# Optimization experiments

Hardware: AMD Instinct MI355X
Metric: run time of the kernel (lower is better)

## Reference

```python
import math
import jax, jax.numpy as jnp
import numpy as np

POS_DIM = 16
MLP_HIDDEN = 32
HIDDEN = 1024


def _pos_emb(n_bins: int, pos_dim: int = POS_DIM) -> jnp.ndarray:
    pos = jnp.arange(n_bins, dtype=jnp.float32)[:, None]            # [n_bins, 1]
    inv_freq = jnp.exp(jnp.arange(0, pos_dim, 2, dtype=jnp.float32)
                       * (-math.log(10000.0) / pos_dim))            # [pos_dim//2]
    pe = jnp.zeros((n_bins, pos_dim), dtype=jnp.float32)
    pe = pe.at[:, 0::2].set(jnp.sin(pos * inv_freq))
    pe = pe.at[:, 1::2].set(jnp.cos(pos * inv_freq))
    return pe


def setup_inputs() -> dict:
    key = jax.random.key(0)
    kx, k1, k2, k3, k4 = jax.random.split(key, 5)
    x = jax.random.normal(kx, (4, 4096, HIDDEN), dtype=jnp.float32)
    # filter MLP params (torch Linear default-ish init scale)
    W1 = jax.random.normal(k1, (POS_DIM, MLP_HIDDEN), dtype=jnp.float32) / math.sqrt(POS_DIM)
    b1 = jax.random.normal(k2, (MLP_HIDDEN,), dtype=jnp.float32) * 0.01
    W2 = jax.random.normal(k3, (MLP_HIDDEN, HIDDEN), dtype=jnp.float32) / math.sqrt(MLP_HIDDEN)
    b2 = jax.random.normal(k4, (HIDDEN,), dtype=jnp.float32) * 0.01
    amp_gain = jnp.ones((HIDDEN,), dtype=jnp.float32)
    return {"x": x, "W1": W1, "b1": b1, "W2": W2, "b2": b2, "amp_gain": amp_gain}


def reference(x, W1, b1, W2, b2, amp_gain):
    B, T, D = x.shape
    n_bins = T // 2 + 1
    pe = _pos_emb(n_bins)                                           # [n_bins, pos_dim]
    # tiny filter MLP: Linear -> SiLU -> Linear
    h = jax.nn.silu(pe @ W1 + b1)                                   # [n_bins, mlp_hidden]
    H = (h @ W2 + b2).astype(jnp.float32)                           # [n_bins, D]
    Xf = jnp.fft.rfft(x.astype(jnp.float32), axis=1)                # [B, n_bins, D] complex
    Yf = Xf * H[None, :, :]
    y = jnp.fft.irfft(Yf, n=T, axis=1)                              # [B, T, D]
    return y.astype(x.dtype) * amp_gain[None, None, :]
```

## Files before the change

### kernel.cpp

```cpp
#include <hip/hip_runtime.h>
#include <hip/hip_bf16.h>
#include <cstddef>


#define B_ 4
#define T_ 4096
#define D_ 1024
#define D2_ 512
#define NBINS 2049

constexpr float WC16[8] = {1.f, 0.9238795325112867f, 0.7071067811865476f,
                           0.3826834323650898f, 0.f, -0.3826834323650898f,
                           -0.7071067811865476f, -0.9238795325112867f};
constexpr float WS16[8] = {0.f, 0.3826834323650898f, 0.7071067811865476f,
                           0.9238795325112867f, 1.f, 0.9238795325112867f,
                           0.7071067811865476f, 0.3826834323650898f};

template <int SGN>
__device__ __forceinline__ void dft16(float (&vr)[16], float (&vi)[16]) {
#pragma unroll
  for (int i = 0; i < 16; ++i) {
    const int j = ((i & 1) << 3) | ((i & 2) << 1) | ((i & 4) >> 1) | ((i & 8) >> 3);
    if (j > i) {
      float t = vr[i]; vr[i] = vr[j]; vr[j] = t;
      t = vi[i]; vi[i] = vi[j]; vi[j] = t;
    }
  }
#pragma unroll
  for (int s = 1; s <= 4; ++s) {
    const int L = 1 << s, hh = L >> 1, step = 16 >> s;
#pragma unroll
    for (int k0 = 0; k0 < 16; k0 += L)
#pragma unroll
      for (int j = 0; j < hh; ++j) {
        const float wr = WC16[j * step];
        const float wi = (float)SGN * WS16[j * step];
        const int ia = k0 + j, ib = ia + hh;
        const float tr = wr * vr[ib] - wi * vi[ib];
        const float ti = wr * vi[ib] + wi * vr[ib];
        vr[ib] = vr[ia] - tr; vi[ib] = vi[ia] - ti;
        vr[ia] += tr; vi[ia] += ti;
      }
  }
}

__device__ __forceinline__ void twiddle(float& xr, float& xi, float ang) {
  float sn, cs;
  __sincosf(ang, &sn, &cs);
  const float r = xr * cs - xi * sn;
  xi = xr * sn + xi * cs;
  xr = r;
}

__global__ void k_filter_h(const float* __restrict__ W1, const float* __restrict__ b1,
                           float* __restrict__ h) {
  const int bin = blockIdx.x * 256 + threadIdx.x;
  if (bin >= NBINS) return;
  constexpr float invf[8] = {1.0f, 0.31622776601683794f, 0.1f, 0.031622776601683794f,
                             0.01f, 3.1622776601683794e-3f, 1.0e-3f, 3.1622776601683794e-4f};
  float pe[16];
#pragma unroll
  for (int i = 0; i < 8; ++i) {
    const float a = (float)bin * invf[i];
    pe[2 * i] = sinf(a);
    pe[2 * i + 1] = cosf(a);
  }
#pragma unroll
  for (int m = 0; m < 32; ++m) {
    float s = b1[m];
#pragma unroll
    for (int i = 0; i < 16; ++i) s += pe[i] * W1[i * 32 + m];
    h[bin * 32 + m] = s / (1.0f + expf(-s));
  }
}

__global__ void k_filter_HT(const float* __restrict__ h, const float* __restrict__ W2,
                            const float* __restrict__ b2, float2* __restrict__ HT) {
  const int bin = blockIdx.x * 256 + threadIdx.x;
  const int g = blockIdx.y;
  if (bin >= NBINS) return;
  float sA = b2[2 * g], sB = b2[2 * g + 1];
#pragma unroll
  for (int m = 0; m < 32; ++m) {
    const float hv = h[bin * 32 + m];
    sA += hv * W2[m * D_ + 2 * g];
    sB += hv * W2[m * D_ + 2 * g + 1];
  }
  constexpr float sc = 0.5f / 4096.0f;
  HT[(size_t)g * NBINS + bin] = make_float2((sA + sB) * sc, (sA - sB) * sc);
}

__global__ __launch_bounds__(256, 8) void k_pack_t(const float2* __restrict__ x2,
                                                   float2* __restrict__ Z) {
  __shared__ float2 tile[64][33];
  const int tid = threadIdx.x;
  const int g0 = blockIdx.x * 32;
  const int t0 = blockIdx.y * 64;
  const int b = blockIdx.z;
#pragma unroll
  for (int it = 0; it < 8; ++it) {
    const int l = tid + 256 * it;
    const int r = l >> 5, c = l & 31;
    tile[r][c] = x2[((size_t)b * T_ + t0 + r) * D2_ + g0 + c];
  }
  __syncthreads();
#pragma unroll
  for (int it = 0; it < 8; ++it) {
    const int l = tid + 256 * it;
    const int gg = l >> 6, tt = l & 63;
    Z[((size_t)b * D2_ + g0 + gg) * T_ + t0 + tt] = tile[tt][gg];
  }
}

__global__ __launch_bounds__(256, 4) void k_fft_fused(float2* __restrict__ Z,
                                                      const float2* __restrict__ HT) {
  __shared__ float2 S[4096];
  const int tid = threadIdx.x;
  const int g = blockIdx.x;
  const int b = blockIdx.y;
  float2* __restrict__ Zrow = Z + ((size_t)b * D2_ + g) * T_;
  const float2* __restrict__ HTg = HT + (size_t)g * NBINS;
  constexpr float C1f = -6.28318530717958647692f / 4096.0f;
  constexpr float C2f = -6.28318530717958647692f / 256.0f;
  constexpr float C1i = 6.28318530717958647692f / 4096.0f;
  constexpr float C2i = 6.28318530717958647692f / 256.0f;

  float vr[16], vi[16];
  {
    const int j = tid;
#pragma unroll
    for (int a = 0; a < 16; ++a) {
      const float2 t = Zrow[j + 256 * a];
      vr[a] = t.x; vi[a] = t.y;
    }
    dft16<-1>(vr, vi);
#pragma unroll
    for (int r = 1; r < 16; ++r) twiddle(vr[r], vi[r], C1f * (float)(r * j));
#pragma unroll
    for (int r = 0; r < 16; ++r) S[256 * r + j] = make_float2(vr[r], vi[r]);
  }
  __syncthreads();
  const int rr = tid >> 4, ii = tid & 15;
  {
#pragma unroll
    for (int a = 0; a < 16; ++a) {
      const float2 t = S[256 * rr + ii + 16 * a];
      vr[a] = t.x; vi[a] = t.y;
    }
    __syncthreads();
    dft16<-1>(vr, vi);
#pragma unroll
    for (int r2 = 1; r2 < 16; ++r2) twiddle(vr[r2], vi[r2], C2f * (float)(r2 * ii));
#pragma unroll
    for (int r2 = 0; r2 < 16; ++r2)
      S[256 * ii + 16 * rr + (r2 ^ ii)] = make_float2(vr[r2], vi[r2]);
  }
  __syncthreads();
  {
#pragma unroll
    for (int i2 = 0; i2 < 16; ++i2) {
      const float2 t = S[256 * i2 + 16 * rr + (ii ^ i2)];
      vr[i2] = t.x; vi[i2] = t.y;
    }
    __syncthreads();
    dft16<-1>(vr, vi);
  }
  float2 hv[16];
  {
#pragma unroll
    for (int s2 = 0; s2 < 16; ++s2) {
      const int k = rr + 16 * ii + 256 * s2;
      const int km = (k <= 2048) ? k : 4096 - k;
      hv[s2] = HTg[km];
    }
#pragma unroll
    for (int s2 = 0; s2 < 16; ++s2)
      S[256 * s2 + 16 * ii + (rr ^ ii)] = make_float2(vr[s2], vi[s2]);
    __syncthreads();
#pragma unroll
    for (int s2 = 0; s2 < 16; ++s2) {
      const int k = rr + 16 * ii + 256 * s2;
      const int kp = (4096 - k) & 4095;
      const int d0 = kp & 15, d1 = (kp >> 4) & 15, d2 = kp >> 8;
      const float2 xp = S[256 * d2 + 16 * d1 + (d0 ^ d1)];
      const float yr = hv[s2].x * vr[s2] + hv[s2].y * xp.x;
      const float yi = hv[s2].x * vi[s2] - hv[s2].y * xp.y;
      vr[s2] = yr; vi[s2] = yi;
    }
  }
  __syncthreads();
  {
    dft16<1>(vr, vi);
#pragma unroll
    for (int j0 = 1; j0 < 16; ++j0) twiddle(vr[j0], vi[j0], C2i * (float)(ii * j0));
#pragma unroll
    for (int j0 = 0; j0 < 16; ++j0)
      S[256 * j0 + 16 * rr + (ii ^ j0)] = make_float2(vr[j0], vi[j0]);
  }
  __syncthreads();
  {
#pragma unroll
    for (int r2 = 0; r2 < 16; ++r2) {
      const float2 t = S[256 * ii + 16 * rr + (r2 ^ ii)];
      vr[r2] = t.x; vi[r2] = t.y;
    }
    __syncthreads();
    dft16<1>(vr, vi);
#pragma unroll
    for (int j1 = 0; j1 < 16; ++j1)
      twiddle(vr[j1], vi[j1], C1i * (float)(rr * (ii + 16 * j1)));
#pragma unroll
    for (int j1 = 0; j1 < 16; ++j1)
      S[256 * rr + ii + 16 * j1] = make_float2(vr[j1], vi[j1]);
  }
  __syncthreads();
  {
    const int j = tid;
#pragma unroll
    for (int r = 0; r < 16; ++r) {
      const float2 t = S[256 * r + j];
      vr[r] = t.x; vi[r] = t.y;
    }
    dft16<1>(vr, vi);
#pragma unroll
    for (int a = 0; a < 16; ++a) Zrow[j + 256 * a] = make_float2(vr[a], vi[a]);
  }
}

__global__ __launch_bounds__(256, 8) void k_unpack_t(const float2* __restrict__ Z,
                                                     const float2* __restrict__ amp2,
                                                     float2* __restrict__ y2) {
  __shared__ float2 tile[64][33];
  const int tid = threadIdx.x;
  const int g0 = blockIdx.x * 32;
  const int t0 = blockIdx.y * 64;
  const int b = blockIdx.z;
#pragma unroll
  for (int it = 0; it < 8; ++it) {
    const int l = tid + 256 * it;
    const int gg = l >> 6, tt = l & 63;
    tile[tt][gg] = Z[((size_t)b * D2_ + g0 + gg) * T_ + t0 + tt];
  }
  __syncthreads();
#pragma unroll
  for (int it = 0; it < 8; ++it) {
    const int l = tid + 256 * it;
    const int r = l >> 5, c = l & 31;
    const float2 t = tile[r][c];
    const float2 av = amp2[g0 + c];
    y2[((size_t)b * T_ + t0 + r) * D2_ + g0 + c] = make_float2(t.x * av.x, t.y * av.y);
  }
}

extern "C" void kernel_launch(void* const* d_in, const int* in_sizes, int n_in,
                              void* d_out, int out_size, void* d_ws, size_t ws_size,
                              hipStream_t stream) {
  const float* x = (const float*)d_in[0];
  const float* W1 = (const float*)d_in[1];
  const float* b1 = (const float*)d_in[2];
  const float* W2 = (const float*)d_in[3];
  const float* b2 = (const float*)d_in[4];
  const float* amp = (const float*)d_in[5];
  float* out = (float*)d_out;

  float2* Z = (float2*)d_ws;
  float2* HT = (float2*)((char*)d_ws + (size_t)B_ * D2_ * T_ * sizeof(float2));
  float* h = (float*)((char*)HT + (size_t)D2_ * NBINS * sizeof(float2));

  k_filter_h<<<dim3((NBINS + 255) / 256), 256, 0, stream>>>(W1, b1, h);
  k_filter_HT<<<dim3((NBINS + 255) / 256, D2_), 256, 0, stream>>>(h, W2, b2, HT);
  k_pack_t<<<dim3(D2_ / 32, T_ / 64, B_), 256, 0, stream>>>((const float2*)x, Z);
  k_fft_fused<<<dim3(D2_, B_), 256, 0, stream>>>(Z, HT);
  k_unpack_t<<<dim3(D2_ / 32, T_ / 64, B_), 256, 0, stream>>>(Z, (const float2*)amp,
                                                              (float2*)out);
}
```

Baseline: 120.3 us.

## Chain twiddle recurrences, pre-permute filter table, reorder FFT grid for filter reuse

Twiddle factors in the FFT stages are now produced by one sincos followed by complex-multiply recurrences, replacing a sincos per element. The filter table is expanded into a per-thread pre-permuted 4096-entry layout so each FFT block reads it with coalesced loads and no index math. The FFT grid is swapped so the four batches sharing a filter row run next to each other, improving cache reuse. The 1/N scale moves into the unpack kernel. The recurrences can accumulate some float rounding error, and the filter table is larger.

New measurement: 155.1 us. 1.29x slower.

```diff
diff --git a/kernel.cpp b/kernel.cpp
--- a/kernel.cpp
+++ b/kernel.cpp
@@ -1,6 +1,7 @@
 #include <hip/hip_runtime.h>
 #include <hip/hip_bf16.h>
 #include <cstddef>
+#include <cstdint>
 
 
 #define B_ 4
@@ -44,12 +45,22 @@
   }
 }
 
-__device__ __forceinline__ void twiddle(float& xr, float& xi, float ang) {
-  float sn, cs;
-  __sincosf(ang, &sn, &cs);
-  const float r = xr * cs - xi * sn;
-  xi = xr * sn + xi * cs;
-  xr = r;
+__device__ __forceinline__ void chain_twiddle(float (&vr)[16], float (&vi)[16],
+                                              int r0, float wc, float ws) {
+  float ar = wc, ai = ws;
+#pragma unroll
+  for (int r = 1; r < 16; ++r) {
+    if (r >= r0) {
+      const float tr = vr[r] * ar - vi[r] * ai;
+      vi[r] = vr[r] * ai + vi[r] * ar;
+      vr[r] = tr;
+    }
+    if (r < 15) {
+      const float nr = ar * wc - ai * ws;
+      const float ni = ar * ws + ai * wc;
+      ar = nr; ai = ni;
+    }
+  }
 }
 
 __global__ void k_filter_h(const float* __restrict__ W1, const float* __restrict__ b1,
@@ -74,20 +85,21 @@
   }
 }
 
-__global__ void k_filter_HT(const float* __restrict__ h, const float* __restrict__ W2,
-                            const float* __restrict__ b2, float2* __restrict__ HT) {
-  const int bin = blockIdx.x * 256 + threadIdx.x;
+__global__ void k_filter_HTS(const float* __restrict__ h, const float* __restrict__ W2,
+                             const float* __restrict__ b2, float2* __restrict__ HTS) {
+  const int q = blockIdx.x * 256 + threadIdx.x;
   const int g = blockIdx.y;
-  if (bin >= NBINS) return;
+  const int tid = q & 255, s2 = q >> 8;
+  const int k = (tid >> 4) + 16 * (tid & 15) + 256 * s2;
+  const int km = (k <= 2048) ? k : 4096 - k;
   float sA = b2[2 * g], sB = b2[2 * g + 1];
 #pragma unroll
   for (int m = 0; m < 32; ++m) {
-    const float hv = h[bin * 32 + m];
+    const float hv = h[km * 32 + m];
     sA += hv * W2[m * D_ + 2 * g];
     sB += hv * W2[m * D_ + 2 * g + 1];
   }
-  constexpr float sc = 0.5f / 4096.0f;
-  HT[(size_t)g * NBINS + bin] = make_float2((sA + sB) * sc, (sA - sB) * sc);
+  HTS[(size_t)g * 4096 + q] = make_float2((sA + sB) * 0.5f, (sA - sB) * 0.5f);
 }
 
 __global__ __launch_bounds__(256, 8) void k_pack_t(const float2* __restrict__ x2,
@@ -113,17 +125,16 @@
 }
 
 __global__ __launch_bounds__(256, 4) void k_fft_fused(float2* __restrict__ Z,
-                                                      const float2* __restrict__ HT) {
+                                                      const float2* __restrict__ HTS) {
   __shared__ float2 S[4096];
   const int tid = threadIdx.x;
-  const int g = blockIdx.x;
-  const int b = blockIdx.y;
+  const int b = blockIdx.x;
+  const int g = blockIdx.y;
   float2* __restrict__ Zrow = Z + ((size_t)b * D2_ + g) * T_;
-  const float2* __restrict__ HTg = HT + (size_t)g * NBINS;
+  const float2* __restrict__ HTSg = HTS + (size_t)g * 4096;
   constexpr float C1f = -6.28318530717958647692f / 4096.0f;
   constexpr float C2f = -6.28318530717958647692f / 256.0f;
   constexpr float C1i = 6.28318530717958647692f / 4096.0f;
-  constexpr float C2i = 6.28318530717958647692f / 256.0f;
 
   float vr[16], vi[16];
   {
@@ -134,13 +145,16 @@
       vr[a] = t.x; vi[a] = t.y;
     }
     dft16<-1>(vr, vi);
-#pragma unroll
-    for (int r = 1; r < 16; ++r) twiddle(vr[r], vi[r], C1f * (float)(r * j));
+    float wc, ws;
+    __sincosf(C1f * (float)j, &ws, &wc);
+    chain_twiddle(vr, vi, 1, wc, ws);
 #pragma unroll
     for (int r = 0; r < 16; ++r) S[256 * r + j] = make_float2(vr[r], vi[r]);
   }
   __syncthreads();
   const int rr = tid >> 4, ii = tid & 15;
+  float w2c, w2s;
+  __sincosf(C2f * (float)ii, &w2s, &w2c);
   {
 #pragma unroll
     for (int a = 0; a < 16; ++a) {
@@ -149,8 +163,7 @@
     }
     __syncthreads();
     dft16<-1>(vr, vi);
-#pragma unroll
-    for (int r2 = 1; r2 < 16; ++r2) twiddle(vr[r2], vi[r2], C2f * (float)(r2 * ii));
+    chain_twiddle(vr, vi, 1, w2c, w2s);
 #pragma unroll
     for (int r2 = 0; r2 < 16; ++r2)
       S[256 * ii + 16 * rr + (r2 ^ ii)] = make_float2(vr[r2], vi[r2]);
@@ -168,11 +181,7 @@
   float2 hv[16];
   {
 #pragma unroll
-    for (int s2 = 0; s2 < 16; ++s2) {
-      const int k = rr + 16 * ii + 256 * s2;
-      const int km = (k <= 2048) ? k : 4096 - k;
-      hv[s2] = HTg[km];
-    }
+    for (int s2 = 0; s2 < 16; ++s2) hv[s2] = HTSg[256 * s2 + tid];
 #pragma unroll
     for (int s2 = 0; s2 < 16; ++s2)
       S[256 * s2 + 16 * ii + (rr ^ ii)] = make_float2(vr[s2], vi[s2]);
@@ -191,8 +200,7 @@
   __syncthreads();
   {
     dft16<1>(vr, vi);
-#pragma unroll
-    for (int j0 = 1; j0 < 16; ++j0) twiddle(vr[j0], vi[j0], C2i * (float)(ii * j0));
+    chain_twiddle(vr, vi, 1, w2c, -w2s);
 #pragma unroll
     for (int j0 = 0; j0 < 16; ++j0)
       S[256 * j0 + 16 * rr + (ii ^ j0)] = make_float2(vr[j0], vi[j0]);
@@ -206,9 +214,21 @@
     }
     __syncthreads();
     dft16<1>(vr, vi);
-#pragma unroll
-    for (int j1 = 0; j1 < 16; ++j1)
-      twiddle(vr[j1], vi[j1], C1i * (float)(rr * (ii + 16 * j1)));
+    float bc, bs, sc, ss;
+    __sincosf(C1i * (float)(rr * ii), &bs, &bc);
+    __sincosf(C1i * (float)(16 * rr), &ss, &sc);
+    float ar = bc, ai = bs;
+#pragma unroll
+    for (int j1 = 0; j1 < 16; ++j1) {
+      const float tr = vr[j1] * ar - vi[j1] * ai;
+      vi[j1] = vr[j1] * ai + vi[j1] * ar;
+      vr[j1] = tr;
+      if (j1 < 15) {
+        const float nr = ar * sc - ai * ss;
+        const float ni = ar * ss + ai * sc;
+        ar = nr; ai = ni;
+      }
+    }
 #pragma unroll
     for (int j1 = 0; j1 < 16; ++j1)
       S[256 * rr + ii + 16 * j1] = make_float2(vr[j1], vi[j1]);
@@ -248,7 +268,9 @@
     const int r = l >> 5, c = l & 31;
     const float2 t = tile[r][c];
     const float2 av = amp2[g0 + c];
-    y2[((size_t)b * T_ + t0 + r) * D2_ + g0 + c] = make_float2(t.x * av.x, t.y * av.y);
+    constexpr float invN = 1.0f / 4096.0f;
+    y2[((size_t)b * T_ + t0 + r) * D2_ + g0 + c] =
+        make_float2(t.x * av.x * invN, t.y * av.y * invN);
   }
 }
 
@@ -264,13 +286,13 @@
   float* out = (float*)d_out;
 
   float2* Z = (float2*)d_ws;
-  float2* HT = (float2*)((char*)d_ws + (size_t)B_ * D2_ * T_ * sizeof(float2));
-  float* h = (float*)((char*)HT + (size_t)D2_ * NBINS * sizeof(float2));
+  float2* HTS = (float2*)((char*)d_ws + (size_t)B_ * D2_ * T_ * sizeof(float2));
+  float* h = (float*)((char*)HTS + (size_t)D2_ * 4096 * sizeof(float2));
 
   k_filter_h<<<dim3((NBINS + 255) / 256), 256, 0, stream>>>(W1, b1, h);
-  k_filter_HT<<<dim3((NBINS + 255) / 256, D2_), 256, 0, stream>>>(h, W2, b2, HT);
+  k_filter_HTS<<<dim3(16, D2_), 256, 0, stream>>>(h, W2, b2, HTS);
   k_pack_t<<<dim3(D2_ / 32, T_ / 64, B_), 256, 0, stream>>>((const float2*)x, Z);
-  k_fft_fused<<<dim3(D2_, B_), 256, 0, stream>>>(Z, HT);
+  k_fft_fused<<<dim3(B_, D2_), 256, 0, stream>>>(Z, HTS);
   k_unpack_t<<<dim3(D2_ / 32, T_ / 64, B_), 256, 0, stream>>>(Z, (const float2*)amp,
                                                               (float2*)out);
 }
```
